# Kernel optimization log

Measured on AMD Instinct MI355X. Metric: run time of the kernel, lower is better.

Reference implementation:

```python
import jax, jax.numpy as jnp
import numpy as np

EPS = 1e-6
N_HEAD, N_KV_HEAD = 16, 4
VE_GATE_CH = 12

def rmsnorm(x):
    return x * jax.lax.rsqrt(jnp.mean(x * x, axis=-1, keepdims=True) + EPS)

def apply_rotary_emb(x, cos, sin):
    half = x.shape[-1] // 2
    x1, x2 = x[..., :half], x[..., half:]
    return jnp.concatenate([x1 * cos + x2 * sin, -x1 * sin + x2 * cos], axis=-1)

def setup_inputs():
    key = jax.random.key(0)
    ks = jax.random.split(key, 8)
    B, S, D = 2, 2048, 1024
    H, KVH = N_HEAD, N_KV_HEAD
    hd = D // H
    x = jax.random.normal(ks[0], (B, S, D), jnp.float32)
    ve = jax.random.normal(ks[1], (B, S, KVH * hd), jnp.float32)
    # real rotary tables, broadcastable over [B,S,H,hd//2]
    inv_freq = 1.0 / (10000.0 ** (np.arange(hd // 2, dtype=np.float32) / (hd // 2)))
    ang = np.arange(S, dtype=np.float32)[:, None] * inv_freq[None, :]  # [S, hd//2]
    cos = jnp.asarray(np.cos(ang))[:, None, :]  # [S,1,hd//2]
    sin = jnp.asarray(np.sin(ang))[:, None, :]
    std = 0.02
    Wq = jax.random.normal(ks[2], (D, H * hd), jnp.float32) * std
    Wk = jax.random.normal(ks[3], (D, KVH * hd), jnp.float32) * std
    Wv = jax.random.normal(ks[4], (D, KVH * hd), jnp.float32) * std
    Wo = jax.random.normal(ks[5], (D, D), jnp.float32) * std
    Wg = jax.random.normal(ks[6], (VE_GATE_CH, KVH), jnp.float32) * std
    return {"x": x, "ve": ve, "cos": cos, "sin": sin, "Wq": Wq, "Wk": Wk,
            "Wv": Wv, "Wo": Wo, "Wg": Wg, "window_size": 512}

def reference(x, ve, cos, sin, Wq, Wk, Wv, Wo, Wg, window_size):
    B, S, D = x.shape
    H, KVH = N_HEAD, N_KV_HEAD
    hd = D // H
    q = (x @ Wq).reshape(B, S, H, hd)
    k = (x @ Wk).reshape(B, S, KVH, hd)
    v = (x @ Wv).reshape(B, S, KVH, hd)
    # value-embedding gating
    gate = 3.0 * jax.nn.sigmoid(x[..., :VE_GATE_CH] @ Wg)  # [B,S,KVH]
    v = v + gate[..., None] * ve.reshape(B, S, KVH, hd)
    # RoPE + QK rmsnorm * 1.2
    q = rmsnorm(apply_rotary_emb(q, cos, sin)) * 1.2
    k = rmsnorm(apply_rotary_emb(k, cos, sin)) * 1.2
    # GQA head repeat (repeat_interleave over head dim)
    rep = H // KVH
    k = jnp.repeat(k, rep, axis=2)  # [B,S,H,hd]
    v = jnp.repeat(v, rep, axis=2)
    scale = 1.0 / np.sqrt(hd).astype(np.float32)
    scores = jnp.einsum('bqhd,bkhd->bhqk', q, k) * scale  # [B,H,S,S]
    pos = jnp.arange(S)
    allow = (pos[None, :] <= pos[:, None]) & (pos[None, :] >= pos[:, None] - window_size + 1)
    scores = jnp.where(allow[None, None], scores, -jnp.inf)
    attn = jax.nn.softmax(scores, axis=-1)
    y = jnp.einsum('bhqk,bkhd->bqhd', attn, v).reshape(B, S, D)
    return y @ Wo
```

## Files before the change

kernel.cpp:

```cpp
#include <hip/hip_runtime.h>
#include <hip/hip_bf16.h>
#include <cstddef>


typedef short v8s __attribute__((ext_vector_type(8)));
typedef float v4f __attribute__((ext_vector_type(4)));

__device__ __forceinline__ ushort f2b(float f) {
  __hip_bfloat16 h = __float2bfloat16(f);
  return reinterpret_cast<ushort&>(h);
}

__global__ __launch_bounds__(256) void cvt_f32_bf16(
    const float* __restrict__ src, ushort* __restrict__ dst, int n)
{
  int i = (blockIdx.x * 256 + threadIdx.x) * 4;
  if (i >= n) return;
  float4 v = *(const float4*)(src + i);
  ushort4 o;
  o.x = f2b(v.x); o.y = f2b(v.y); o.z = f2b(v.z); o.w = f2b(v.w);
  *(ushort4*)(dst + i) = o;
}

__global__ __launch_bounds__(256) void transpose_cvt4(
    const float* __restrict__ Wq, const float* __restrict__ Wk,
    const float* __restrict__ Wv, const float* __restrict__ Wo,
    ushort* __restrict__ Wqt, ushort* __restrict__ Wkt,
    ushort* __restrict__ Wvt, ushort* __restrict__ Wot)
{
  __shared__ ushort tile[32][33];
  const int z = blockIdx.z;
  const float* W = (z == 0) ? Wq : (z == 1) ? Wo : (z == 2) ? Wk : Wv;
  ushort* Wt     = (z == 0) ? Wqt : (z == 1) ? Wot : (z == 2) ? Wkt : Wvt;
  const int N = (z < 2) ? 1024 : 256;
  const int n0 = blockIdx.x * 32, k0 = blockIdx.y * 32;
  if (n0 >= N) return;
  const int tx = threadIdx.x & 31, ty = threadIdx.x >> 5;
#pragma unroll
  for (int i = 0; i < 4; ++i) {
    const int k = ty + i * 8;
    tile[k][tx] = f2b(W[(size_t)(k0 + k) * N + n0 + tx]);
  }
  __syncthreads();
#pragma unroll
  for (int i = 0; i < 4; ++i) {
    const int n = ty + i * 8;
    Wt[(size_t)(n0 + n) * 1024 + k0 + tx] = tile[tx][n];
  }
}

__global__ __launch_bounds__(256) void gemm_bf16nt(
    const ushort* __restrict__ A, const ushort* __restrict__ Bt,
    float* __restrict__ C, int N, int K)
{
  __shared__ ushort As[128][72];
  __shared__ ushort Bs[128][72];
  const int m0 = blockIdx.x * 128, n0 = blockIdx.y * 128;
  const int t = threadIdx.x;
  const int lane = t & 63, wave = t >> 6;
  const int wr = wave >> 1, wc = wave & 1;
  const int quad = lane >> 4, l16 = lane & 15;

  v4f acc[4][4];
#pragma unroll
  for (int i = 0; i < 4; ++i)
#pragma unroll
    for (int j = 0; j < 4; ++j) acc[i][j] = (v4f){0.f, 0.f, 0.f, 0.f};

  const int row0 = t >> 3, oct = t & 7;
  for (int k0 = 0; k0 < K; k0 += 64) {
#pragma unroll
    for (int i = 0; i < 4; ++i) {
      const int row = row0 + i * 32;
      *(int4*)&As[row][oct * 8] = *(const int4*)(A  + (size_t)(m0 + row) * K + k0 + oct * 8);
      *(int4*)&Bs[row][oct * 8] = *(const int4*)(Bt + (size_t)(n0 + row) * K + k0 + oct * 8);
    }
    __syncthreads();
#pragma unroll
    for (int ks = 0; ks < 2; ++ks) {
      v8s af[4], bf[4];
#pragma unroll
      for (int i = 0; i < 4; ++i) {
        af[i] = *(const v8s*)&As[wr * 64 + i * 16 + l16][ks * 32 + quad * 8];
        bf[i] = *(const v8s*)&Bs[wc * 64 + i * 16 + l16][ks * 32 + quad * 8];
      }
#pragma unroll
      for (int mt = 0; mt < 4; ++mt)
#pragma unroll
        for (int nt = 0; nt < 4; ++nt)
          acc[mt][nt] = __builtin_amdgcn_mfma_f32_16x16x32_bf16(
              af[mt], bf[nt], acc[mt][nt], 0, 0, 0);
    }
    __syncthreads();
  }
#pragma unroll
  for (int mt = 0; mt < 4; ++mt)
#pragma unroll
    for (int r = 0; r < 4; ++r) {
      float* cp = C + (size_t)(m0 + wr * 64 + mt * 16 + quad * 4 + r) * N
                    + n0 + wc * 64 + l16;
#pragma unroll
      for (int nt = 0; nt < 4; ++nt) cp[nt * 16] = acc[mt][nt][r];
    }
}

__global__ __launch_bounds__(256) void postproc(
    const float* __restrict__ qkv, const float* __restrict__ x,
    const float* __restrict__ ve, const float* __restrict__ cosp,
    const float* __restrict__ sinp, const float* __restrict__ Wg,
    ushort* __restrict__ qb, ushort* __restrict__ kb, ushort* __restrict__ vtb)
{
  const int bs = blockIdx.x;
  const int s = bs & 2047, b = bs >> 11;
  const int t = threadIdx.x;
  const int wave = t >> 6, lane = t & 63;
  const int j = lane & 31;
  const float c  = cosp[s * 32 + j];
  const float sn = sinp[s * 32 + j];
  const float* row = qkv + (size_t)bs * 1536;

  for (int task = wave; task < 24; task += 4) {
    if (task < 16) {
      float val = row[task * 64 + lane];
      float other = __shfl_xor(val, 32);
      float rot = (lane < 32) ? (val * c + other * sn) : (val * c - other * sn);
      float ss = rot * rot;
#pragma unroll
      for (int m = 1; m < 64; m <<= 1) ss += __shfl_xor(ss, m);
      float rs = rsqrtf(ss * (1.0f / 64.0f) + 1e-6f) * 1.2f;
      qb[(size_t)bs * 1024 + task * 64 + lane] = f2b(rot * rs);
    } else if (task < 20) {
      const int hk = task - 16;
      float val = row[1024 + hk * 64 + lane];
      float other = __shfl_xor(val, 32);
      float rot = (lane < 32) ? (val * c + other * sn) : (val * c - other * sn);
      float ss = rot * rot;
#pragma unroll
      for (int m = 1; m < 64; m <<= 1) ss += __shfl_xor(ss, m);
      float rs = rsqrtf(ss * (1.0f / 64.0f) + 1e-6f) * 1.2f;
      kb[(size_t)bs * 256 + hk * 64 + lane] = f2b(rot * rs);
    } else {
      const int kvh = task - 20;
      float g = 0.f;
#pragma unroll
      for (int i = 0; i < 12; ++i) g += x[(size_t)bs * 1024 + i] * Wg[i * 4 + kvh];
      const float gate = 3.0f / (1.0f + __expf(-g));
      const float v = row[1280 + kvh * 64 + lane] + gate * ve[(size_t)bs * 256 + kvh * 64 + lane];
      vtb[((size_t)((b * 4 + kvh) * 64 + lane)) * 2048 + s] = f2b(v);
    }
  }
}

__global__ __launch_bounds__(256) void attn_mfma(
    const ushort* __restrict__ qb, const ushort* __restrict__ kb,
    const ushort* __restrict__ vtb, ushort* __restrict__ yb,
    const int* __restrict__ wptr)
{
  __shared__ ushort Ks[64][72];
  __shared__ ushort Vt[80][72];
  __shared__ ushort Ps[128][72];
  const int qt = blockIdx.x, h = blockIdx.y, b = blockIdx.z;
  const int kvh = h >> 2, q0 = qt * 128;
  const int t = threadIdx.x, lane = t & 63, wave = t >> 6;
  const int quad = lane >> 4, l16 = lane & 15;
  const int Wwin = *wptr;

  v8s qf[2][2];
#pragma unroll
  for (int s = 0; s < 2; ++s) {
    const ushort* qp = qb + ((size_t)(b * 2048 + q0 + wave * 32 + s * 16 + l16)) * 1024
                          + h * 64 + quad * 8;
    qf[s][0] = *(const v8s*)qp;
    qf[s][1] = *(const v8s*)(qp + 32);
  }

  if (t < 128) {
    const int row = 64 + (t >> 3), c8 = (t & 7) * 8;
    const int v = (row == 64) ? 0x3F803F80 : 0;
    int4 w; w.x = v; w.y = v; w.z = v; w.w = v;
    *(int4*)&Vt[row][c8] = w;
  }

  v4f o[2][5];
#pragma unroll
  for (int s = 0; s < 2; ++s)
#pragma unroll
    for (int d = 0; d < 5; ++d) o[s][d] = (v4f){0.f, 0.f, 0.f, 0.f};

  const int lo = q0 - Wwin + 1;
  const int kt0 = (lo > 0) ? (lo >> 6) : 0;
  const int kt1 = (q0 + 127) >> 6;

  for (int kt = kt0; kt <= kt1; ++kt) {
#pragma unroll
    for (int i = 0; i < 2; ++i) {
      const int cc = t + i * 256;
      const int r8 = cc >> 3, c8 = (cc & 7) * 8;
      *(int4*)&Ks[r8][c8] =
          *(const int4*)(kb + ((size_t)(b * 2048 + kt * 64 + r8)) * 256 + kvh * 64 + c8);
      *(int4*)&Vt[r8][c8] =
          *(const int4*)(vtb + ((size_t)((b * 4 + kvh) * 64 + r8)) * 2048 + kt * 64 + c8);
    }
    __syncthreads();

    const bool needs_mask = (kt * 64 + 63 > q0) || (kt * 64 < q0 + 128 - Wwin);

#pragma unroll
    for (int s = 0; s < 2; ++s) {
      const int qrow = q0 + wave * 32 + s * 16 + l16;
      ushort* prow = &Ps[wave * 32 + s * 16 + l16][0];
#pragma unroll
      for (int nt = 0; nt < 4; ++nt) {
        v8s kf0 = *(const v8s*)&Ks[nt * 16 + l16][quad * 8];
        v8s kf1 = *(const v8s*)&Ks[nt * 16 + l16][32 + quad * 8];
        v4f st = (v4f){0.f, 0.f, 0.f, 0.f};
        st = __builtin_amdgcn_mfma_f32_16x16x32_bf16(kf0, qf[s][0], st, 0, 0, 0);
        st = __builtin_amdgcn_mfma_f32_16x16x32_bf16(kf1, qf[s][1], st, 0, 0, 0);
        float p[4];
#pragma unroll
        for (int r = 0; r < 4; ++r) {
          p[r] = __expf(fmaf(st[r], 0.125f, -12.0f));
          if (needs_mask) {
            const int k = kt * 64 + nt * 16 + quad * 4 + r;
            const bool ok = (k <= qrow) && (k > qrow - Wwin);
            p[r] = ok ? p[r] : 0.0f;
          }
        }
        uint2 w;
        w.x = (uint)f2b(p[0]) | ((uint)f2b(p[1]) << 16);
        w.y = (uint)f2b(p[2]) | ((uint)f2b(p[3]) << 16);
        *(uint2*)(prow + nt * 16 + quad * 4) = w;
      }
    }

    v8s pf[2][2];
#pragma unroll
    for (int s = 0; s < 2; ++s) {
      pf[s][0] = *(const v8s*)&Ps[wave * 32 + s * 16 + l16][quad * 8];
      pf[s][1] = *(const v8s*)&Ps[wave * 32 + s * 16 + l16][32 + quad * 8];
    }
#pragma unroll
    for (int dt = 0; dt < 5; ++dt) {
      v8s vf0 = *(const v8s*)&Vt[dt * 16 + l16][quad * 8];
      v8s vf1 = *(const v8s*)&Vt[dt * 16 + l16][32 + quad * 8];
#pragma unroll
      for (int s = 0; s < 2; ++s) {
        o[s][dt] = __builtin_amdgcn_mfma_f32_16x16x32_bf16(pf[s][0], vf0, o[s][dt], 0, 0, 0);
        o[s][dt] = __builtin_amdgcn_mfma_f32_16x16x32_bf16(pf[s][1], vf1, o[s][dt], 0, 0, 0);
      }
    }
    __syncthreads();
  }

#pragma unroll
  for (int s = 0; s < 2; ++s)
#pragma unroll
    for (int r = 0; r < 4; ++r) {
      const float l = __shfl(o[s][4][r], lane & 48);
      const float inv = 1.0f / l;
      ushort* yp = yb + ((size_t)(b * 2048 + q0 + wave * 32 + s * 16 + quad * 4 + r)) * 1024
                      + h * 64 + l16;
#pragma unroll
      for (int dt = 0; dt < 4; ++dt) yp[dt * 16] = f2b(o[s][dt][r] * inv);
    }
}

extern "C" void kernel_launch(void* const* d_in, const int* in_sizes, int n_in,
                              void* d_out, int out_size, void* d_ws, size_t ws_size,
                              hipStream_t stream)
{
  const float* x    = (const float*)d_in[0];
  const float* ve   = (const float*)d_in[1];
  const float* cosp = (const float*)d_in[2];
  const float* sinp = (const float*)d_in[3];
  const float* Wq   = (const float*)d_in[4];
  const float* Wk   = (const float*)d_in[5];
  const float* Wv   = (const float*)d_in[6];
  const float* Wo   = (const float*)d_in[7];
  const float* Wg   = (const float*)d_in[8];
  const int*   win  = (const int*)d_in[9];
  float* out = (float*)d_out;

  char* p = (char*)d_ws;
  float*  qkvws = (float*)p;   p += (size_t)4096 * 1536 * 4;
  ushort* xb    = (ushort*)p;  p += (size_t)4194304 * 2;
  ushort* kb    = (ushort*)p;  p += (size_t)1048576 * 2;
  ushort* vtb   = (ushort*)p;  p += (size_t)1048576 * 2;
  ushort* Wqkvt = (ushort*)p;  p += (size_t)1536 * 1024 * 2;
  ushort* Wot   = (ushort*)p;
  ushort* qb = xb;
  ushort* yb = (ushort*)qkvws;

  cvt_f32_bf16<<<4096, 256, 0, stream>>>(x, xb, 4194304);
  transpose_cvt4<<<dim3(32, 32, 4), 256, 0, stream>>>(
      Wq, Wk, Wv, Wo,
      Wqkvt, Wqkvt + (size_t)1024 * 1024, Wqkvt + (size_t)1280 * 1024, Wot);

  gemm_bf16nt<<<dim3(32, 12), 256, 0, stream>>>(xb, Wqkvt, qkvws, 1536, 1024);

  postproc<<<dim3(4096), 256, 0, stream>>>(qkvws, x, ve, cosp, sinp, Wg, qb, kb, vtb);

  attn_mfma<<<dim3(16, 16, 2), 256, 0, stream>>>(qb, kb, vtb, yb, win);

  gemm_bf16nt<<<dim3(32, 8), 256, 0, stream>>>(yb, Wot, out, 1024, 1024);
}
```

Baseline: 188.5 us.

## Fuse RoPE/RMSNorm/gating into QKV GEMM epilogue and use async LDS loads

The QKV GEMM epilogue now applies RoPE, QK RMSNorm and value-embedding gating directly from accumulators, writing bf16 q/k/v. This removes the fp32 QKV round trip and the separate postproc kernel. V is transposed by a small tiled kernel, and the gates are computed during the x conversion. The GEMM main loop switches to global_load_lds async copies into unpadded LDS tiles, which may add bank conflicts on the MFMA fragment reads.

```diff
diff --git a/kernel.cpp b/kernel.cpp
--- a/kernel.cpp
+++ b/kernel.cpp
@@ -1,6 +1,7 @@
 #include <hip/hip_runtime.h>
 #include <hip/hip_bf16.h>
 #include <cstddef>
+#include <cstdint>
 
 
 typedef short v8s __attribute__((ext_vector_type(8)));
@@ -11,15 +12,36 @@
   return reinterpret_cast<ushort&>(h);
 }
 
-__global__ __launch_bounds__(256) void cvt_f32_bf16(
-    const float* __restrict__ src, ushort* __restrict__ dst, int n)
-{
-  int i = (blockIdx.x * 256 + threadIdx.x) * 4;
-  if (i >= n) return;
-  float4 v = *(const float4*)(src + i);
+__device__ __forceinline__ void async16(const ushort* g, ushort* l) {
+  __builtin_amdgcn_global_load_lds(
+      (__attribute__((address_space(1))) void*)(uintptr_t)(const void*)g,
+      (__attribute__((address_space(3))) void*)(uintptr_t)(void*)l, 16, 0, 0);
+}
+
+__global__ __launch_bounds__(256) void cvt_gate(
+    const float* __restrict__ x, ushort* __restrict__ xb,
+    const float* __restrict__ Wg, float* __restrict__ gates)
+{
+  const int bs = blockIdx.x, t = threadIdx.x;
+  const float* row = x + (size_t)bs * 1024;
+  float4 v = *(const float4*)(row + t * 4);
   ushort4 o;
   o.x = f2b(v.x); o.y = f2b(v.y); o.z = f2b(v.z); o.w = f2b(v.w);
-  *(ushort4*)(dst + i) = o;
+  *(ushort4*)(xb + (size_t)bs * 1024 + t * 4) = o;
+  if (t < 4) {
+    float g = 0.f;
+#pragma unroll
+    for (int i = 0; i < 12; ++i) g += row[i] * Wg[i * 4 + t];
+    gates[bs * 4 + t] = 3.0f / (1.0f + __expf(-g));
+  }
+}
+
+__global__ __launch_bounds__(256) void prep_cs(
+    const float* __restrict__ cosp, const float* __restrict__ sinp,
+    float2* __restrict__ cs)
+{
+  const int i = blockIdx.x * 256 + threadIdx.x;
+  cs[i] = make_float2(cosp[i], sinp[i]);
 }
 
 __global__ __launch_bounds__(256) void transpose_cvt4(
@@ -49,31 +71,35 @@
   }
 }
 
-__global__ __launch_bounds__(256) void gemm_bf16nt(
+__device__ __forceinline__ void gemm_mainloop(
     const ushort* __restrict__ A, const ushort* __restrict__ Bt,
-    float* __restrict__ C, int N, int K)
-{
-  __shared__ ushort As[128][72];
-  __shared__ ushort Bs[128][72];
-  const int m0 = blockIdx.x * 128, n0 = blockIdx.y * 128;
+    int K, int m0, int n0, ushort (*As)[64], ushort (*Bs)[64],
+    v4f acc[4][4])
+{
   const int t = threadIdx.x;
   const int lane = t & 63, wave = t >> 6;
   const int wr = wave >> 1, wc = wave & 1;
   const int quad = lane >> 4, l16 = lane & 15;
-
-  v4f acc[4][4];
-#pragma unroll
-  for (int i = 0; i < 4; ++i)
-#pragma unroll
-    for (int j = 0; j < 4; ++j) acc[i][j] = (v4f){0.f, 0.f, 0.f, 0.f};
-
-  const int row0 = t >> 3, oct = t & 7;
+  const int l8 = lane >> 3, c8 = (lane & 7) * 8;
+
+  const ushort* ap[4];
+  const ushort* bp[4];
+  ushort* al[4];
+  ushort* bl[4];
+#pragma unroll
+  for (int i = 0; i < 4; ++i) {
+    const int row = (wave * 4 + i) * 8 + l8;
+    ap[i] = A  + (size_t)(m0 + row) * K + c8;
+    bp[i] = Bt + (size_t)(n0 + row) * K + c8;
+    al[i] = &As[(wave * 4 + i) * 8][0];
+    bl[i] = &Bs[(wave * 4 + i) * 8][0];
+  }
+
   for (int k0 = 0; k0 < K; k0 += 64) {
 #pragma unroll
     for (int i = 0; i < 4; ++i) {
-      const int row = row0 + i * 32;
-      *(int4*)&As[row][oct * 8] = *(const int4*)(A  + (size_t)(m0 + row) * K + k0 + oct * 8);
-      *(int4*)&Bs[row][oct * 8] = *(const int4*)(Bt + (size_t)(n0 + row) * K + k0 + oct * 8);
+      async16(ap[i] + k0, al[i]);
+      async16(bp[i] + k0, bl[i]);
     }
     __syncthreads();
 #pragma unroll
@@ -93,61 +119,129 @@
     }
     __syncthreads();
   }
+}
+
+__global__ __launch_bounds__(256) void gemm_qkv_fused(
+    const ushort* __restrict__ A, const ushort* __restrict__ Bt,
+    const float2* __restrict__ cs, const float* __restrict__ gates,
+    const float* __restrict__ ve,
+    ushort* __restrict__ qb, ushort* __restrict__ kb, ushort* __restrict__ vb)
+{
+  __shared__ ushort As[128][64];
+  __shared__ ushort Bs[128][64];
+  const int m0 = blockIdx.x * 128, n0 = blockIdx.y * 128;
+  const int lane = threadIdx.x & 63, wave = threadIdx.x >> 6;
+  const int wr = wave >> 1, wc = wave & 1;
+  const int quad = lane >> 4, l16 = lane & 15;
+
+  v4f acc[4][4];
+#pragma unroll
+  for (int i = 0; i < 4; ++i)
+#pragma unroll
+    for (int j = 0; j < 4; ++j) acc[i][j] = (v4f){0.f, 0.f, 0.f, 0.f};
+
+  gemm_mainloop(A, Bt, 1024, m0, n0, As, Bs, acc);
+
+  const int sec = blockIdx.y;
+  const int head_col = n0 + wc * 64;
+
+  if (sec < 10) {
+    const bool isQ = (sec < 8);
+    const int h = (head_col - (isQ ? 0 : 1024)) >> 6;
+    ushort* dst = isQ ? qb : kb;
+    const int ld = isQ ? 1024 : 256;
+#pragma unroll
+    for (int mt = 0; mt < 4; ++mt)
+#pragma unroll
+      for (int r = 0; r < 4; ++r) {
+        const int row = m0 + wr * 64 + mt * 16 + quad * 4 + r;
+        const int s = row & 2047;
+        const float2 cs0 = cs[s * 32 + l16];
+        const float2 cs1 = cs[s * 32 + 16 + l16];
+        const float x10 = acc[mt][0][r], x11 = acc[mt][1][r];
+        const float x20 = acc[mt][2][r], x21 = acc[mt][3][r];
+        float ss = x10 * x10 + x11 * x11 + x20 * x20 + x21 * x21;
+        ss += __shfl_xor(ss, 1);
+        ss += __shfl_xor(ss, 2);
+        ss += __shfl_xor(ss, 4);
+        ss += __shfl_xor(ss, 8);
+        const float rs = rsqrtf(ss * (1.0f / 64.0f) + 1e-6f) * 1.2f;
+        ushort* dp = dst + (size_t)row * ld + h * 64 + l16;
+        dp[0]  = f2b((x10 * cs0.x + x20 * cs0.y) * rs);
+        dp[16] = f2b((x11 * cs1.x + x21 * cs1.y) * rs);
+        dp[32] = f2b((-x10 * cs0.y + x20 * cs0.x) * rs);
+        dp[48] = f2b((-x11 * cs1.y + x21 * cs1.x) * rs);
+      }
+  } else {
+    const int kvh = (head_col - 1280) >> 6;
+#pragma unroll
+    for (int mt = 0; mt < 4; ++mt)
+#pragma unroll
+      for (int r = 0; r < 4; ++r) {
+        const int row = m0 + wr * 64 + mt * 16 + quad * 4 + r;
+        const float gate = gates[row * 4 + kvh];
+        const float* vep = ve + (size_t)row * 256 + kvh * 64 + l16;
+        ushort* dp = vb + (size_t)row * 256 + kvh * 64 + l16;
+#pragma unroll
+        for (int nt = 0; nt < 4; ++nt)
+          dp[nt * 16] = f2b(acc[mt][nt][r] + gate * vep[nt * 16]);
+      }
+  }
+}
+
+__global__ __launch_bounds__(256) void gemm_wo(
+    const ushort* __restrict__ A, const ushort* __restrict__ Bt,
+    float* __restrict__ C)
+{
+  __shared__ ushort As[128][64];
+  __shared__ ushort Bs[128][64];
+  const int m0 = blockIdx.x * 128, n0 = blockIdx.y * 128;
+  const int lane = threadIdx.x & 63, wave = threadIdx.x >> 6;
+  const int wr = wave >> 1, wc = wave & 1;
+  const int quad = lane >> 4, l16 = lane & 15;
+
+  v4f acc[4][4];
+#pragma unroll
+  for (int i = 0; i < 4; ++i)
+#pragma unroll
+    for (int j = 0; j < 4; ++j) acc[i][j] = (v4f){0.f, 0.f, 0.f, 0.f};
+
+  gemm_mainloop(A, Bt, 1024, m0, n0, As, Bs, acc);
+
 #pragma unroll
   for (int mt = 0; mt < 4; ++mt)
 #pragma unroll
     for (int r = 0; r < 4; ++r) {
-      float* cp = C + (size_t)(m0 + wr * 64 + mt * 16 + quad * 4 + r) * N
+      float* cp = C + (size_t)(m0 + wr * 64 + mt * 16 + quad * 4 + r) * 1024
                     + n0 + wc * 64 + l16;
 #pragma unroll
       for (int nt = 0; nt < 4; ++nt) cp[nt * 16] = acc[mt][nt][r];
     }
 }
 
-__global__ __launch_bounds__(256) void postproc(
-    const float* __restrict__ qkv, const float* __restrict__ x,
-    const float* __restrict__ ve, const float* __restrict__ cosp,
-    const float* __restrict__ sinp, const float* __restrict__ Wg,
-    ushort* __restrict__ qb, ushort* __restrict__ kb, ushort* __restrict__ vtb)
-{
-  const int bs = blockIdx.x;
-  const int s = bs & 2047, b = bs >> 11;
+__global__ __launch_bounds__(256) void transpose_v(
+    const ushort* __restrict__ vb, ushort* __restrict__ vtb)
+{
+  __shared__ ushort L[64][72];
+  const int s0 = blockIdx.x * 64, kvh = blockIdx.y, b = blockIdx.z;
   const int t = threadIdx.x;
-  const int wave = t >> 6, lane = t & 63;
-  const int j = lane & 31;
-  const float c  = cosp[s * 32 + j];
-  const float sn = sinp[s * 32 + j];
-  const float* row = qkv + (size_t)bs * 1536;
-
-  for (int task = wave; task < 24; task += 4) {
-    if (task < 16) {
-      float val = row[task * 64 + lane];
-      float other = __shfl_xor(val, 32);
-      float rot = (lane < 32) ? (val * c + other * sn) : (val * c - other * sn);
-      float ss = rot * rot;
-#pragma unroll
-      for (int m = 1; m < 64; m <<= 1) ss += __shfl_xor(ss, m);
-      float rs = rsqrtf(ss * (1.0f / 64.0f) + 1e-6f) * 1.2f;
-      qb[(size_t)bs * 1024 + task * 64 + lane] = f2b(rot * rs);
-    } else if (task < 20) {
-      const int hk = task - 16;
-      float val = row[1024 + hk * 64 + lane];
-      float other = __shfl_xor(val, 32);
-      float rot = (lane < 32) ? (val * c + other * sn) : (val * c - other * sn);
-      float ss = rot * rot;
-#pragma unroll
-      for (int m = 1; m < 64; m <<= 1) ss += __shfl_xor(ss, m);
-      float rs = rsqrtf(ss * (1.0f / 64.0f) + 1e-6f) * 1.2f;
-      kb[(size_t)bs * 256 + hk * 64 + lane] = f2b(rot * rs);
-    } else {
-      const int kvh = task - 20;
-      float g = 0.f;
-#pragma unroll
-      for (int i = 0; i < 12; ++i) g += x[(size_t)bs * 1024 + i] * Wg[i * 4 + kvh];
-      const float gate = 3.0f / (1.0f + __expf(-g));
-      const float v = row[1280 + kvh * 64 + lane] + gate * ve[(size_t)bs * 256 + kvh * 64 + lane];
-      vtb[((size_t)((b * 4 + kvh) * 64 + lane)) * 2048 + s] = f2b(v);
-    }
+#pragma unroll
+  for (int i = 0; i < 2; ++i) {
+    const int cc = t + i * 256;
+    const int srow = cc >> 3, c8 = (cc & 7) * 8;
+    *(int4*)&L[srow][c8] =
+        *(const int4*)(vb + ((size_t)(b * 2048 + s0 + srow)) * 256 + kvh * 64 + c8);
+  }
+  __syncthreads();
+#pragma unroll
+  for (int i = 0; i < 2; ++i) {
+    const int cc = t + i * 256;
+    const int drow = cc >> 3, s8 = (cc & 7) * 8;
+    ushort w[8];
+#pragma unroll
+    for (int jj = 0; jj < 8; ++jj) w[jj] = L[s8 + jj][drow];
+    *(int4*)(vtb + ((size_t)((b * 4 + kvh) * 64 + drow)) * 2048 + s0 + s8) =
+        *(int4*)w;
   }
 }
 
@@ -282,25 +376,28 @@
   float* out = (float*)d_out;
 
   char* p = (char*)d_ws;
-  float*  qkvws = (float*)p;   p += (size_t)4096 * 1536 * 4;
   ushort* xb    = (ushort*)p;  p += (size_t)4194304 * 2;
+  ushort* qb    = (ushort*)p;  p += (size_t)4194304 * 2;
+  ushort* yb    = (ushort*)p;  p += (size_t)4194304 * 2;
   ushort* kb    = (ushort*)p;  p += (size_t)1048576 * 2;
+  ushort* vb    = (ushort*)p;  p += (size_t)1048576 * 2;
   ushort* vtb   = (ushort*)p;  p += (size_t)1048576 * 2;
   ushort* Wqkvt = (ushort*)p;  p += (size_t)1536 * 1024 * 2;
-  ushort* Wot   = (ushort*)p;
-  ushort* qb = xb;
-  ushort* yb = (ushort*)qkvws;
-
-  cvt_f32_bf16<<<4096, 256, 0, stream>>>(x, xb, 4194304);
+  ushort* Wot   = (ushort*)p;  p += (size_t)1048576 * 2;
+  float2* cs    = (float2*)p;  p += (size_t)65536 * 8;
+  float*  gates = (float*)p;
+
+  cvt_gate<<<4096, 256, 0, stream>>>(x, xb, Wg, gates);
+  prep_cs<<<256, 256, 0, stream>>>(cosp, sinp, cs);
   transpose_cvt4<<<dim3(32, 32, 4), 256, 0, stream>>>(
       Wq, Wk, Wv, Wo,
       Wqkvt, Wqkvt + (size_t)1024 * 1024, Wqkvt + (size_t)1280 * 1024, Wot);
 
-  gemm_bf16nt<<<dim3(32, 12), 256, 0, stream>>>(xb, Wqkvt, qkvws, 1536, 1024);
-
-  postproc<<<dim3(4096), 256, 0, stream>>>(qkvws, x, ve, cosp, sinp, Wg, qb, kb, vtb);
+  gemm_qkv_fused<<<dim3(32, 12), 256, 0, stream>>>(xb, Wqkvt, cs, gates, ve,
+                                                   qb, kb, vb);
+  transpose_v<<<dim3(32, 4, 2), 256, 0, stream>>>(vb, vtb);
 
   attn_mfma<<<dim3(16, 16, 2), 256, 0, stream>>>(qb, kb, vtb, yb, win);
 
-  gemm_bf16nt<<<dim3(32, 8), 256, 0, stream>>>(yb, Wot, out, 1024, 1024);
-}
+  gemm_wo<<<dim3(32, 8), 256, 0, stream>>>(yb, Wot, out);
+}
```

Measured after the change: 177.5 us. 1.06x faster.
